# Kernel tuning notes

Hardware: AMD Instinct MI355X
Metric: run time of the kernel (lower is better)

## Reference

```python
import jax, jax.numpy as jnp
import numpy as np

B, R, SR, K, F = 1, 4096, 40, 8, 32
H = 256           # shading_feature_num
NVF = 4           # num_viewdir_freqs -> 2*4*3 = 24 PE channels
EPS = 1e-8


def positional_encoding(x, n_freqs):
    # x: [..., 3] -> [..., 2*n_freqs*3]
    freqs = (2.0 ** jnp.arange(n_freqs)).astype(x.dtype)          # [nf]
    ang = x[..., None, :] * freqs[:, None]                        # [..., nf, 3]
    enc = jnp.concatenate([jnp.sin(ang), jnp.cos(ang)], axis=-1)  # [..., nf, 6]
    return enc.reshape(x.shape[:-1] + (2 * n_freqs * 3,))


def setup_inputs() -> dict:
    key = jax.random.key(0)
    ks = jax.random.split(key, 20)
    s = 0.02
    inp = {
        "sampled_embedding": jax.random.normal(ks[0], (B, R, SR, K, F), jnp.float32),
        "dists": jax.random.normal(ks[1], (B, R, SR, K, 3), jnp.float32),
        "viewdirs": jax.random.normal(ks[2], (B, R, SR, 3), jnp.float32),
        "pnt_mask": jax.random.randint(ks[3], (B, R, SR, K), 0, 2, jnp.int32),
        # block1: Linear(F,H), Linear(H,H)
        "W1a": jax.random.normal(ks[4], (F, H), jnp.float32) * s,
        "b1a": jnp.zeros((H,), jnp.float32),
        "W1b": jax.random.normal(ks[5], (H, H), jnp.float32) * s,
        "b1b": jnp.zeros((H,), jnp.float32),
        # block3: Linear(H,H), Linear(H,H)
        "W3a": jax.random.normal(ks[6], (H, H), jnp.float32) * s,
        "b3a": jnp.zeros((H,), jnp.float32),
        "W3b": jax.random.normal(ks[7], (H, H), jnp.float32) * s,
        "b3b": jnp.zeros((H,), jnp.float32),
        # alpha branch: Linear(H,1)
        "Wa": jax.random.normal(ks[8], (H, 1), jnp.float32) * s,
        "ba": jnp.zeros((1,), jnp.float32),
        # color branch: Linear(H + 24, 3)
        "Wc": jax.random.normal(ks[9], (H + 2 * NVF * 3, 3), jnp.float32) * s,
        "bc": jnp.zeros((3,), jnp.float32),
    }
    return inp


def reference(sampled_embedding, dists, viewdirs, pnt_mask,
              W1a, b1a, W1b, b1b, W3a, b3a, W3b, b3b, Wa, ba, Wc, bc):
    mask = pnt_mask.astype(sampled_embedding.dtype)               # [B,R,SR,K]
    # quadric distance kernel: w = mask / max(||d||^2, eps)
    d2 = jnp.sum(dists * dists, axis=-1)                          # [B,R,SR,K]
    w = mask / jnp.maximum(d2, EPS)
    # agg_weight_norm: normalize over neighbors
    w = w / jnp.maximum(jnp.sum(w, axis=-1, keepdims=True), EPS)
    # agg_intrp_order == 0: interpolate features first
    feat = jnp.einsum('brsk,brskf->brsf', w, sampled_embedding)   # [B,R,SR,F]
    h = jax.nn.relu(feat @ W1a + b1a)
    h = jax.nn.relu(h @ W1b + b1b)
    h = jax.nn.relu(h @ W3a + b3a)
    h = jax.nn.relu(h @ W3b + b3b)
    # alpha branch + raw2out_density (act_super=1 -> softplus(x-1))
    alpha = jax.nn.softplus(h @ Wa + ba - 1.0)                    # [B,R,SR,1]
    # color branch: concat viewdir PE, then raw2out_color
    vd = viewdirs / jnp.maximum(jnp.linalg.norm(viewdirs, axis=-1, keepdims=True), EPS)
    vpe = positional_encoding(vd, NVF)                            # [B,R,SR,24]
    raw_c = jnp.concatenate([h, vpe], axis=-1) @ Wc + bc          # [B,R,SR,3]
    color = jax.nn.sigmoid(raw_c) * (1.0 + 2e-3) - 1e-3
    return jnp.concatenate([alpha, color], axis=-1)               # [B,R,SR,4]
```

## Files before the change

kernel.cpp:

```cpp
#include <hip/hip_runtime.h>
#include <hip/hip_bf16.h>
#include <cstdint>

typedef __attribute__((ext_vector_type(8))) short short8;
typedef __attribute__((ext_vector_type(4))) float floatx4;
typedef __attribute__((ext_vector_type(4))) float fx4;
typedef __attribute__((ext_vector_type(4))) uint ux4;

#define ROWS 128
#define NTHREADS 256
#define RSTRIDE 296

#define BAR_PLAIN asm volatile("s_barrier" ::: "memory")
#define BAR_LGKM  asm volatile("s_waitcnt lgkmcnt(0)\n\ts_barrier" ::: "memory")

__device__ __forceinline__ ushort f2bf(float x) {
  union { float f; uint32_t u; } v; v.f = x;
  uint32_t r = v.u + 0x7fffu + ((v.u >> 16) & 1u);
  return (ushort)(r >> 16);
}

__device__ __forceinline__ uint32_t cvtpk2(float lo, float hi) {
  uint32_t r;
  asm("v_cvt_pk_bf16_f32 %0, %1, %2" : "=v"(r) : "v"(lo), "v"(hi));
  return r;
}

__global__ void prep_kernel(const float* __restrict__ W1a, const float* __restrict__ W1b,
                            const float* __restrict__ W3a, const float* __restrict__ W3b,
                            const float* __restrict__ Wa,  const float* __restrict__ Wc,
                            const float* __restrict__ ba,  const float* __restrict__ bc,
                            ushort* __restrict__ W1aT, ushort* __restrict__ W1bT,
                            ushort* __restrict__ W3aT, ushort* __restrict__ W3bT,
                            ushort* __restrict__ whead, float* __restrict__ hbias)
{
  int b = blockIdx.x, t = threadIdx.x;
  W1bT[t * 256 + b] = f2bf(W1b[b * 256 + t]);
  W3aT[t * 256 + b] = f2bf(W3a[b * 256 + t]);
  W3bT[t * 256 + b] = f2bf(W3b[b * 256 + t]);
  if (b < 32) W1aT[t * 32 + b] = f2bf(W1a[b * 256 + t]);
  if (b == 255) {
    for (int k = t; k < 288; k += 256) {
      for (int r = 0; r < 16; ++r) {
        float v = 0.f;
        if (r == 0)     v = (k < 256) ? Wa[k] : 0.f;
        else if (r < 4) v = (k < 280) ? Wc[k * 3 + (r - 1)] : 0.f;
        whead[r * 288 + k] = f2bf(v);
      }
    }
    if (t == 0) { hbias[0] = ba[0]; hbias[1] = bc[0]; hbias[2] = bc[1]; hbias[3] = bc[2]; }
  }
}

__device__ __forceinline__ void phaseA_compute(
    const float* __restrict__ emb, const float* __restrict__ dists,
    const float* __restrict__ viewdirs, const int* __restrict__ pnt_mask,
    int gs, int g, ux4& u0, ux4& u1, ux4& u2, ux4& u3)
{
  float d[24];
  const float4* d4 = (const float4*)(dists + (size_t)gs * 24);
  #pragma unroll
  for (int i = 0; i < 6; ++i) {
    float4 q = d4[i];
    d[4*i] = q.x; d[4*i+1] = q.y; d[4*i+2] = q.z; d[4*i+3] = q.w;
  }
  const int4* m4 = (const int4*)(pnt_mask + (size_t)gs * 8);
  int4 m0 = m4[0], m1 = m4[1];
  int mk[8] = {m0.x, m0.y, m0.z, m0.w, m1.x, m1.y, m1.z, m1.w};
  float wv[8]; float sum = 0.f;
  #pragma unroll
  for (int k = 0; k < 8; ++k) {
    float d2 = d[3*k]*d[3*k] + d[3*k+1]*d[3*k+1] + d[3*k+2]*d[3*k+2];
    wv[k] = (float)mk[k] * __builtin_amdgcn_rcpf(fmaxf(d2, 1e-8f));
    sum += wv[k];
  }
  float inv = __builtin_amdgcn_rcpf(fmaxf(sum, 1e-8f));
  #pragma unroll
  for (int k = 0; k < 8; ++k) wv[k] *= inv;

  float acc[16];
  #pragma unroll
  for (int j = 0; j < 16; ++j) acc[j] = 0.f;
  #pragma unroll
  for (int k = 0; k < 8; ++k) {
    const fx4* e4 = (const fx4*)(emb + ((size_t)(gs * 8 + k)) * 32 + g * 16);
    fx4 e0 = __builtin_nontemporal_load(e4);
    fx4 e1 = __builtin_nontemporal_load(e4 + 1);
    fx4 e2 = __builtin_nontemporal_load(e4 + 2);
    fx4 e3 = __builtin_nontemporal_load(e4 + 3);
    acc[0]  += wv[k]*e0.x; acc[1]  += wv[k]*e0.y; acc[2]  += wv[k]*e0.z; acc[3]  += wv[k]*e0.w;
    acc[4]  += wv[k]*e1.x; acc[5]  += wv[k]*e1.y; acc[6]  += wv[k]*e1.z; acc[7]  += wv[k]*e1.w;
    acc[8]  += wv[k]*e2.x; acc[9]  += wv[k]*e2.y; acc[10] += wv[k]*e2.z; acc[11] += wv[k]*e2.w;
    acc[12] += wv[k]*e3.x; acc[13] += wv[k]*e3.y; acc[14] += wv[k]*e3.z; acc[15] += wv[k]*e3.w;
  }
  u0.x = cvtpk2(acc[0],  acc[1]);  u0.y = cvtpk2(acc[2],  acc[3]);
  u0.z = cvtpk2(acc[4],  acc[5]);  u0.w = cvtpk2(acc[6],  acc[7]);
  u1.x = cvtpk2(acc[8],  acc[9]);  u1.y = cvtpk2(acc[10], acc[11]);
  u1.z = cvtpk2(acc[12], acc[13]); u1.w = cvtpk2(acc[14], acc[15]);

  float vx = viewdirs[(size_t)gs * 3 + 0];
  float vy = viewdirs[(size_t)gs * 3 + 1];
  float vz = viewdirs[(size_t)gs * 3 + 2];
  float nrm = sqrtf(vx*vx + vy*vy + vz*vz);
  float ninv = __builtin_amdgcn_rcpf(fmaxf(nrm, 1e-8f));
  uint32_t pd[6];
  #pragma unroll
  for (int h = 0; h < 2; ++h) {
    float fr = (float)(1 << (2 * g + h)) * ninv;
    float sx, cx, sy, cy, sz, cz;
    sincosf(vx * fr, &sx, &cx);
    sincosf(vy * fr, &sy, &cy);
    sincosf(vz * fr, &sz, &cz);
    pd[3*h + 0] = cvtpk2(sx, sy);
    pd[3*h + 1] = cvtpk2(sz, cx);
    pd[3*h + 2] = cvtpk2(cy, cz);
  }
  u2.x = pd[0]; u2.y = pd[1]; u2.z = pd[2]; u2.w = pd[3];
  u3.x = pd[4]; u3.y = pd[5]; u3.z = 0u;    u3.w = 0u;
}

template<int NKT, int KST, int NKST>
__device__ __forceinline__ void mlp_layer(ushort (*buf)[RSTRIDE],
                                          const ushort* __restrict__ WT,
                                          const ushort* __restrict__ nextWT,
                                          const float* __restrict__ bias,
                                          int mbase, int lrow, int kgrp,
                                          short8 (&a)[4])
{
  floatx4 acc[4][8] = {};
  __builtin_amdgcn_s_setprio(1);
  #pragma unroll
  for (int kt = 0; kt < NKT; ++kt) {
    short8 an[4];
    #pragma unroll
    for (int mt = 0; mt < 4; ++mt) {
      const ushort* src = (kt + 1 < NKT)
        ? &WT[(size_t)(mbase + mt * 16 + lrow) * KST + (kt + 1) * 32 + kgrp * 8]
        : &nextWT[(size_t)(mbase + mt * 16 + lrow) * NKST + kgrp * 8];
      an[mt] = *(const short8*)src;
    }
    short8 b[8];
    #pragma unroll
    for (int nt = 0; nt < 8; ++nt)
      b[nt] = *(const short8*)&buf[nt * 16 + lrow][kt * 32 + kgrp * 8];
    #pragma unroll
    for (int mt = 0; mt < 4; ++mt)
      #pragma unroll
      for (int nt = 0; nt < 8; ++nt)
        acc[mt][nt] = __builtin_amdgcn_mfma_f32_16x16x32_bf16(a[mt], b[nt], acc[mt][nt], 0, 0, 0);
    #pragma unroll
    for (int mt = 0; mt < 4; ++mt) a[mt] = an[mt];
  }
  __builtin_amdgcn_s_setprio(0);
  BAR_PLAIN;
  #pragma unroll
  for (int mt = 0; mt < 4; ++mt) {
    float4 bv = *(const float4*)(bias + mbase + mt * 16 + kgrp * 4);
    #pragma unroll
    for (int nt = 0; nt < 8; ++nt) {
      uint2 pk;
      pk.x = cvtpk2(fmaxf(acc[mt][nt][0] + bv.x, 0.f), fmaxf(acc[mt][nt][1] + bv.y, 0.f));
      pk.y = cvtpk2(fmaxf(acc[mt][nt][2] + bv.z, 0.f), fmaxf(acc[mt][nt][3] + bv.w, 0.f));
      *(uint2*)&buf[nt * 16 + lrow][mbase + mt * 16 + kgrp * 4] = pk;
    }
  }
  BAR_LGKM;
}

__global__ __launch_bounds__(NTHREADS, 2) void pa_fused(
    const float* __restrict__ emb, const float* __restrict__ dists,
    const float* __restrict__ viewdirs, const int* __restrict__ pnt_mask,
    const ushort* __restrict__ W1aT, const float* __restrict__ b1a,
    const ushort* __restrict__ W1bT, const float* __restrict__ b1b,
    const ushort* __restrict__ W3aT, const float* __restrict__ b3a,
    const ushort* __restrict__ W3bT, const float* __restrict__ b3b,
    const ushort* __restrict__ whead, const float* __restrict__ hbias,
    float* __restrict__ out)
{
  __shared__ ushort buf[ROWS][RSTRIDE];
  const int tid  = threadIdx.x;
  const int base = blockIdx.x * ROWS;

  const int lane = tid & 63;
  const int wid  = tid >> 6;
  const int lrow = lane & 15;
  const int kgrp = lane >> 4;
  const int mbase = wid * 64;

  short8 a[4];
  #pragma unroll
  for (int mt = 0; mt < 4; ++mt)
    a[mt] = *(const short8*)&W1aT[(size_t)(mbase + mt * 16 + lrow) * 32 + kgrp * 8];

  {
    const int s = tid >> 1, g = tid & 1;
    ux4 u0, u1, u2, u3;
    phaseA_compute(emb, dists, viewdirs, pnt_mask, base + s, g, u0, u1, u2, u3);
    *(ux4*)&buf[s][g * 16]     = u0;
    *(ux4*)&buf[s][g * 16 + 8] = u1;
    uint2* pe = (uint2*)&buf[s][256 + g * 12];
    pe[0] = make_uint2(u2.x, u2.y);
    pe[1] = make_uint2(u2.z, u2.w);
    pe[2] = make_uint2(u3.x, u3.y);
    if (g == 1) {
      ux4 z = {0, 0, 0, 0};
      *(ux4*)&buf[s][280] = z;
    }
  }
  BAR_LGKM;

  mlp_layer<1, 32, 256>(buf, W1aT, W1bT, b1a, mbase, lrow, kgrp, a);
  mlp_layer<8, 256, 256>(buf, W1bT, W3aT, b1b, mbase, lrow, kgrp, a);
  mlp_layer<8, 256, 256>(buf, W3aT, W3bT, b3a, mbase, lrow, kgrp, a);
  mlp_layer<8, 256, 256>(buf, W3bT, W3bT, b3b, mbase, lrow, kgrp, a);

  __builtin_amdgcn_s_setprio(1);
  #pragma unroll
  for (int h = 0; h < 2; ++h) {
    floatx4 hacc = {0.f, 0.f, 0.f, 0.f};
    #pragma unroll
    for (int kt = 0; kt < 9; ++kt) {
      short8 ah = *(const short8*)&whead[(size_t)lrow * 288 + kt * 32 + kgrp * 8];
      short8 b = *(const short8*)&buf[wid * 32 + h * 16 + lrow][kt * 32 + kgrp * 8];
      hacc = __builtin_amdgcn_mfma_f32_16x16x32_bf16(ah, b, hacc, 0, 0, 0);
    }
    if (lane < 16) {
      float4 hb = *(const float4*)hbias;
      float ra = hacc[0] + hb.x - 1.f;
      float alpha = fmaxf(ra, 0.f) + log1pf(expf(-fabsf(ra)));
      float c0 = hacc[1] + hb.y, c1 = hacc[2] + hb.z, c2 = hacc[3] + hb.w;
      fx4 o;
      o.x = alpha;
      o.y = 1.f / (1.f + expf(-c0)) * 1.002f - 1e-3f;
      o.z = 1.f / (1.f + expf(-c1)) * 1.002f - 1e-3f;
      o.w = 1.f / (1.f + expf(-c2)) * 1.002f - 1e-3f;
      int gs = base + wid * 32 + h * 16 + lane;
      __builtin_nontemporal_store(o, (fx4*)(out + (size_t)gs * 4));
    }
  }
  __builtin_amdgcn_s_setprio(0);
}

extern "C" void kernel_launch(void* const* d_in, const int* in_sizes, int n_in,
                              void* d_out, int out_size, void* d_ws, size_t ws_size,
                              hipStream_t stream)
{
  const float* emb   = (const float*)d_in[0];
  const float* dists = (const float*)d_in[1];
  const float* vdirs = (const float*)d_in[2];
  const int*   mask  = (const int*)d_in[3];
  const float* W1a = (const float*)d_in[4];
  const float* b1a = (const float*)d_in[5];
  const float* W1b = (const float*)d_in[6];
  const float* b1b = (const float*)d_in[7];
  const float* W3a = (const float*)d_in[8];
  const float* b3a = (const float*)d_in[9];
  const float* W3b = (const float*)d_in[10];
  const float* b3b = (const float*)d_in[11];
  const float* Wa  = (const float*)d_in[12];
  const float* ba  = (const float*)d_in[13];
  const float* Wc  = (const float*)d_in[14];
  const float* bc  = (const float*)d_in[15];

  int nsamples = in_sizes[2] / 3;

  ushort* wsb  = (ushort*)d_ws;
  ushort* W1aT  = wsb;
  ushort* W1bT  = wsb + 8192;
  ushort* W3aT  = wsb + 73728;
  ushort* W3bT  = wsb + 139264;
  ushort* whead = wsb + 204800;
  float*  hbias = (float*)(wsb + 209408);

  prep_kernel<<<256, 256, 0, stream>>>(W1a, W1b, W3a, W3b, Wa, Wc, ba, bc,
                                       W1aT, W1bT, W3aT, W3bT, whead, hbias);

  int nblocks = nsamples / ROWS;
  pa_fused<<<nblocks, NTHREADS, 0, stream>>>(emb, dists, vdirs, mask,
                                             W1aT, b1a, W1bT, b1b, W3aT, b3a, W3bT, b3b,
                                             whead, hbias, (float*)d_out);
}
```

Before: 134.5 us.

## Switch MLP layers to 32x32x16 bf16 MFMA tiles with LDS B prefetch

Each MLP layer now uses 32x32x16 bf16 MFMA instructions on 2x4 tiles of 32x32 instead of 4x8 tiles of 16x16x32. This halves the number of B-operand LDS reads per output and lowers MFMA issue count. It also double-buffers both the weight and activation fragments inside the k loop. The cross-layer weight prefetch is dropped, so each layer starts with an exposed global load of its weights. The epilogue is rewritten for the 32x32 accumulator layout.

Measured after the change: 131.1 us. 1.03x faster.

```diff
diff --git a/kernel.cpp b/kernel.cpp
--- a/kernel.cpp
+++ b/kernel.cpp
@@ -4,6 +4,7 @@
 
 typedef __attribute__((ext_vector_type(8))) short short8;
 typedef __attribute__((ext_vector_type(4))) float floatx4;
+typedef __attribute__((ext_vector_type(16))) float floatx16;
 typedef __attribute__((ext_vector_type(4))) float fx4;
 typedef __attribute__((ext_vector_type(4))) uint ux4;
 
@@ -119,49 +120,59 @@
   u3.x = pd[4]; u3.y = pd[5]; u3.z = 0u;    u3.w = 0u;
 }
 
-template<int NKT, int KST, int NKST>
-__device__ __forceinline__ void mlp_layer(ushort (*buf)[RSTRIDE],
-                                          const ushort* __restrict__ WT,
-                                          const ushort* __restrict__ nextWT,
-                                          const float* __restrict__ bias,
-                                          int mbase, int lrow, int kgrp,
-                                          short8 (&a)[4])
-{
-  floatx4 acc[4][8] = {};
+template<int NKT, int KST>
+__device__ __forceinline__ void mlp_layer32(ushort (*buf)[RSTRIDE],
+                                            const ushort* __restrict__ WT,
+                                            const float* __restrict__ bias,
+                                            int mbase, int l31, int kh)
+{
+  floatx16 acc[2][4] = {};
+  const ushort* wp = WT + (size_t)(mbase + l31) * KST + kh * 8;
+  short8 a[2], b[4];
+  #pragma unroll
+  for (int mt = 0; mt < 2; ++mt)
+    a[mt] = *(const short8*)(wp + (size_t)mt * 32 * KST);
+  #pragma unroll
+  for (int nt = 0; nt < 4; ++nt)
+    b[nt] = *(const short8*)&buf[nt * 32 + l31][kh * 8];
   __builtin_amdgcn_s_setprio(1);
   #pragma unroll
   for (int kt = 0; kt < NKT; ++kt) {
-    short8 an[4];
-    #pragma unroll
-    for (int mt = 0; mt < 4; ++mt) {
-      const ushort* src = (kt + 1 < NKT)
-        ? &WT[(size_t)(mbase + mt * 16 + lrow) * KST + (kt + 1) * 32 + kgrp * 8]
-        : &nextWT[(size_t)(mbase + mt * 16 + lrow) * NKST + kgrp * 8];
-      an[mt] = *(const short8*)src;
-    }
-    short8 b[8];
-    #pragma unroll
-    for (int nt = 0; nt < 8; ++nt)
-      b[nt] = *(const short8*)&buf[nt * 16 + lrow][kt * 32 + kgrp * 8];
-    #pragma unroll
-    for (int mt = 0; mt < 4; ++mt)
+    int ktn = (kt + 1 < NKT) ? (kt + 1) : 0;
+    short8 an[2], bn[4];
+    #pragma unroll
+    for (int mt = 0; mt < 2; ++mt)
+      an[mt] = *(const short8*)(wp + (size_t)mt * 32 * KST + ktn * 16);
+    #pragma unroll
+    for (int nt = 0; nt < 4; ++nt)
+      bn[nt] = *(const short8*)&buf[nt * 32 + l31][ktn * 16 + kh * 8];
+    #pragma unroll
+    for (int mt = 0; mt < 2; ++mt)
       #pragma unroll
-      for (int nt = 0; nt < 8; ++nt)
-        acc[mt][nt] = __builtin_amdgcn_mfma_f32_16x16x32_bf16(a[mt], b[nt], acc[mt][nt], 0, 0, 0);
-    #pragma unroll
-    for (int mt = 0; mt < 4; ++mt) a[mt] = an[mt];
+      for (int nt = 0; nt < 4; ++nt)
+        acc[mt][nt] = __builtin_amdgcn_mfma_f32_32x32x16_bf16(a[mt], b[nt], acc[mt][nt], 0, 0, 0);
+    #pragma unroll
+    for (int mt = 0; mt < 2; ++mt) a[mt] = an[mt];
+    #pragma unroll
+    for (int nt = 0; nt < 4; ++nt) b[nt] = bn[nt];
   }
   __builtin_amdgcn_s_setprio(0);
   BAR_PLAIN;
-  #pragma unroll
-  for (int mt = 0; mt < 4; ++mt) {
-    float4 bv = *(const float4*)(bias + mbase + mt * 16 + kgrp * 4);
-    #pragma unroll
-    for (int nt = 0; nt < 8; ++nt) {
-      uint2 pk;
-      pk.x = cvtpk2(fmaxf(acc[mt][nt][0] + bv.x, 0.f), fmaxf(acc[mt][nt][1] + bv.y, 0.f));
-      pk.y = cvtpk2(fmaxf(acc[mt][nt][2] + bv.z, 0.f), fmaxf(acc[mt][nt][3] + bv.w, 0.f));
-      *(uint2*)&buf[nt * 16 + lrow][mbase + mt * 16 + kgrp * 4] = pk;
+  const int hi4 = kh * 4;
+  #pragma unroll
+  for (int mt = 0; mt < 2; ++mt) {
+    #pragma unroll
+    for (int q = 0; q < 4; ++q) {
+      float4 bv = *(const float4*)(bias + mbase + mt * 32 + q * 8 + hi4);
+      #pragma unroll
+      for (int nt = 0; nt < 4; ++nt) {
+        uint2 pk;
+        pk.x = cvtpk2(fmaxf(acc[mt][nt][4*q]   + bv.x, 0.f),
+                      fmaxf(acc[mt][nt][4*q+1] + bv.y, 0.f));
+        pk.y = cvtpk2(fmaxf(acc[mt][nt][4*q+2] + bv.z, 0.f),
+                      fmaxf(acc[mt][nt][4*q+3] + bv.w, 0.f));
+        *(uint2*)&buf[nt * 32 + l31][mbase + mt * 32 + q * 8 + hi4] = pk;
+      }
     }
   }
   BAR_LGKM;
@@ -183,14 +194,9 @@
 
   const int lane = tid & 63;
   const int wid  = tid >> 6;
-  const int lrow = lane & 15;
-  const int kgrp = lane >> 4;
+  const int l31  = lane & 31;
+  const int kh   = lane >> 5;
   const int mbase = wid * 64;
-
-  short8 a[4];
-  #pragma unroll
-  for (int mt = 0; mt < 4; ++mt)
-    a[mt] = *(const short8*)&W1aT[(size_t)(mbase + mt * 16 + lrow) * 32 + kgrp * 8];
 
   {
     const int s = tid >> 1, g = tid & 1;
@@ -209,11 +215,13 @@
   }
   BAR_LGKM;
 
-  mlp_layer<1, 32, 256>(buf, W1aT, W1bT, b1a, mbase, lrow, kgrp, a);
-  mlp_layer<8, 256, 256>(buf, W1bT, W3aT, b1b, mbase, lrow, kgrp, a);
-  mlp_layer<8, 256, 256>(buf, W3aT, W3bT, b3a, mbase, lrow, kgrp, a);
-  mlp_layer<8, 256, 256>(buf, W3bT, W3bT, b3b, mbase, lrow, kgrp, a);
-
+  mlp_layer32<2, 32>(buf, W1aT, b1a, mbase, l31, kh);
+  mlp_layer32<16, 256>(buf, W1bT, b1b, mbase, l31, kh);
+  mlp_layer32<16, 256>(buf, W3aT, b3a, mbase, l31, kh);
+  mlp_layer32<16, 256>(buf, W3bT, b3b, mbase, l31, kh);
+
+  const int lrow = lane & 15;
+  const int kgrp = lane >> 4;
   __builtin_amdgcn_s_setprio(1);
   #pragma unroll
   for (int h = 0; h < 2; ++h) {
@@ -221,8 +229,8 @@
     #pragma unroll
     for (int kt = 0; kt < 9; ++kt) {
       short8 ah = *(const short8*)&whead[(size_t)lrow * 288 + kt * 32 + kgrp * 8];
-      short8 b = *(const short8*)&buf[wid * 32 + h * 16 + lrow][kt * 32 + kgrp * 8];
-      hacc = __builtin_amdgcn_mfma_f32_16x16x32_bf16(ah, b, hacc, 0, 0, 0);
+      short8 bh = *(const short8*)&buf[wid * 32 + h * 16 + lrow][kt * 32 + kgrp * 8];
+      hacc = __builtin_amdgcn_mfma_f32_16x16x32_bf16(ah, bh, hacc, 0, 0, 0);
     }
     if (lane < 16) {
       float4 hb = *(const float4*)hbias;
```
